# Performance work log

Measured on AMD Instinct MI355X. Metric: run time of the kernel, lower is better.

The kernel has to match this reference:

```python
import jax, jax.numpy as jnp
import numpy as np

B, S, D, H = 2, 2048, 1024, 16
HD = D // H
EPS = 1e-5


def layer_norm(x, g, b):
    mu = jnp.mean(x, axis=-1, keepdims=True)
    var = jnp.mean(jnp.square(x - mu), axis=-1, keepdims=True)
    return (x - mu) * jax.lax.rsqrt(var + EPS) * g + b


def setup_inputs() -> dict:
    key = jax.random.key(0)
    ks = jax.random.split(key, 10)
    s = 0.02
    return {
        'x': jax.random.normal(ks[0], (B, S, D), jnp.float32),
        'Wq': jax.random.normal(ks[1], (D, D), jnp.float32) * s,
        'bq': jnp.zeros((D,), jnp.float32),
        'Wk': jax.random.normal(ks[2], (D, D), jnp.float32) * s,
        'bk': jnp.zeros((D,), jnp.float32),
        'Wv': jax.random.normal(ks[3], (D, D), jnp.float32) * s,
        'bv': jnp.zeros((D,), jnp.float32),
        'W1': jax.random.normal(ks[4], (D, 4 * D), jnp.float32) * s,
        'b1': jnp.zeros((4 * D,), jnp.float32),
        'W2': jax.random.normal(ks[5], (4 * D, D), jnp.float32) * s,
        'b2': jnp.zeros((D,), jnp.float32),
        'g1': jnp.ones((D,), jnp.float32),
        'be1': jnp.zeros((D,), jnp.float32),
        'g2': jnp.ones((D,), jnp.float32),
        'be2': jnp.zeros((D,), jnp.float32),
    }


def reference(x, Wq, bq, Wk, bk, Wv, bv, W1, b1, W2, b2, g1, be1, g2, be2):
    b, s, d = x.shape
    # QKV projections, split heads: [B,H,S,HD]
    Q = (x @ Wq + bq).reshape(b, s, H, HD).transpose(0, 2, 1, 3)
    K = (x @ Wk + bk).reshape(b, s, H, HD).transpose(0, 2, 1, 3)
    V = (x @ Wv + bv).reshape(b, s, H, HD).transpose(0, 2, 1, 3)
    score = jnp.einsum('bhqd,bhkd->bhqk', Q, K) / jnp.sqrt(jnp.float32(HD))
    attn = jax.nn.softmax(score, axis=-1)
    out = jnp.einsum('bhqk,bhkd->bhqd', attn, V)
    out = out.transpose(0, 2, 1, 3).reshape(b, s, d)
    # dropout(p=0.1) is identity in eval mode
    out = layer_norm(out + x, g1, be1)
    ffn = jax.nn.gelu(out @ W1 + b1, approximate=False) @ W2 + b2
    # NOTE: faithful to source: norm2(output + output), i.e. 2*ffn_out
    return layer_norm(ffn + ffn, g2, be2)
```

## Files before the change

kernel.cpp:

```cpp
#include <hip/hip_runtime.h>
#include <hip/hip_bf16.h>

typedef __hip_bfloat16 bf16;
typedef __attribute__((ext_vector_type(8))) short short8;
typedef __attribute__((ext_vector_type(4))) float floatx4;

struct __align__(8) bf16x4 { bf16 v[4]; };

#define LOG2E 1.4426950408889634f

__device__ __forceinline__ void gload_lds16(const void* g, void* l) {
  __builtin_amdgcn_global_load_lds(
      (const __attribute__((address_space(1))) void*)g,
      (__attribute__((address_space(3))) void*)l, 16, 0, 0);
}

__device__ __forceinline__ floatx4 mfma16(short8 a, short8 b, floatx4 c) {
  return __builtin_amdgcn_mfma_f32_16x16x32_bf16(a, b, c, 0, 0, 0);
}

__global__ __launch_bounds__(256) void convert_x(const float* __restrict__ x,
                                                 bf16* __restrict__ xb) {
  int i = blockIdx.x * 256 + threadIdx.x;
  float4 v = ((const float4*)x)[i];
  bf16x4 o;
  o.v[0] = __float2bfloat16(v.x);
  o.v[1] = __float2bfloat16(v.y);
  o.v[2] = __float2bfloat16(v.z);
  o.v[3] = __float2bfloat16(v.w);
  ((bf16x4*)xb)[i] = o;
}

__global__ __launch_bounds__(256) void transpose_w(const float* __restrict__ W,
                                                   bf16* __restrict__ WT,
                                                   int K, int N) {
  __shared__ float t[64][65];
  const int n0 = blockIdx.x * 64, k0 = blockIdx.y * 64;
  const int tid = threadIdx.x;
#pragma unroll
  for (int i = 0; i < 16; ++i) {
    int idx = i * 256 + tid;
    int r = idx >> 6, c = idx & 63;
    t[r][c] = W[(size_t)(k0 + r) * N + n0 + c];
  }
  __syncthreads();
#pragma unroll
  for (int i = 0; i < 16; ++i) {
    int idx = i * 256 + tid;
    int r = idx >> 6, c = idx & 63;
    WT[(size_t)(n0 + r) * K + k0 + c] = __float2bfloat16(t[c][r]);
  }
}

__global__ __launch_bounds__(256) void transpose_v(const bf16* __restrict__ V,
                                                   bf16* __restrict__ Vt) {
  __shared__ bf16 t[64][72];
  const int bh = blockIdx.y;
  const int s0 = blockIdx.x * 64;
  const bf16* src = V + (size_t)bh * 2048 * 64;
  bf16* dst = Vt + (size_t)bh * 64 * 2048;
  const int tid = threadIdx.x;
#pragma unroll
  for (int i = 0; i < 16; ++i) {
    int idx = i * 256 + tid;
    int r = idx >> 6, c = idx & 63;
    t[r][c] = src[(size_t)(s0 + r) * 64 + c];
  }
  __syncthreads();
#pragma unroll
  for (int i = 0; i < 16; ++i) {
    int idx = i * 256 + tid;
    int r = idx >> 6, c = idx & 63;
    dst[(size_t)r * 2048 + s0 + c] = t[c][r];
  }
}

template <int MODE>
__global__ __launch_bounds__(512, 2) void gemm256(
    const bf16* __restrict__ A, const bf16* __restrict__ BT,
    const float* __restrict__ bias0, const float* __restrict__ bias1,
    const float* __restrict__ bias2, void* __restrict__ C0,
    void* __restrict__ C1, void* __restrict__ C2,
    int M, int N, int K, int lda, int ldb) {
  __shared__ bf16 As[2][256 * 64];
  __shared__ bf16 Bs[2][256 * 64];
  const int tid = threadIdx.x;
  const int lane = tid & 63, wid = tid >> 6;
  const int l16 = lane & 15, lhi = lane >> 4;
  const int wm = wid >> 2, wn = wid & 3;
  const int nwg = gridDim.x * gridDim.y;
  const int orig = blockIdx.y * gridDim.x + blockIdx.x;
  const int wflat = (orig & 7) * (nwg >> 3) + (orig >> 3);
  const int bx = wflat % gridDim.x, by = wflat / gridDim.x;
  const int brow = by * 256, bcol = bx * 256;
  const int swz = (l16 & 7) << 4;
  floatx4 acc[8][4] = {};

  auto stage = [&](int buf, int kt) {
#pragma unroll
    for (int i = 0; i < 4; ++i) {
      const int f = i * 512 + tid;
      const int row = f >> 3;
      const int cb = ((f & 7) * 16) ^ ((row & 7) << 4);
      gload_lds16((const char*)A + ((size_t)(brow + row) * lda + kt) * 2 + cb,
                  (char*)&As[buf][0] + (size_t)f * 16);
    }
#pragma unroll
    for (int i = 0; i < 4; ++i) {
      const int f = i * 512 + tid;
      const int row = f >> 3;
      const int cb = ((f & 7) * 16) ^ ((row & 7) << 4);
      gload_lds16((const char*)BT + ((size_t)(bcol + row) * ldb + kt) * 2 + cb,
                  (char*)&Bs[buf][0] + (size_t)f * 16);
    }
  };

  const int nk = K >> 6;
  stage(0, 0);
  asm volatile("s_waitcnt vmcnt(0)" ::: "memory");
  asm volatile("s_barrier" ::: "memory");
  int cur = 0;
  for (int t = 0; t < nk; ++t) {
    const char* Ab = (const char*)&As[cur][0];
    const char* Bb = (const char*)&Bs[cur][0];
    short8 af[8], b0, b1;
#pragma unroll
    for (int m = 0; m < 8; ++m)
      af[m] = *(const short8*)(Ab + (wm * 128 + m * 16 + l16) * 128 + ((lhi * 16) ^ swz));
    b0 = *(const short8*)(Bb + (wn * 64 + l16) * 128 + ((lhi * 16) ^ swz));
    b1 = *(const short8*)(Bb + (wn * 64 + 16 + l16) * 128 + ((lhi * 16) ^ swz));
    if (t + 1 < nk) stage(cur ^ 1, (t + 1) << 6);
    asm volatile("s_barrier" ::: "memory");
    __builtin_amdgcn_s_setprio(1);
#pragma unroll
    for (int m = 0; m < 8; ++m) {
      acc[m][0] = mfma16(af[m], b0, acc[m][0]);
      acc[m][1] = mfma16(af[m], b1, acc[m][1]);
    }
    __builtin_amdgcn_s_setprio(0);
    asm volatile("s_barrier" ::: "memory");
    b0 = *(const short8*)(Bb + (wn * 64 + 32 + l16) * 128 + ((lhi * 16) ^ swz));
    b1 = *(const short8*)(Bb + (wn * 64 + 48 + l16) * 128 + ((lhi * 16) ^ swz));
    asm volatile("s_barrier" ::: "memory");
    __builtin_amdgcn_s_setprio(1);
#pragma unroll
    for (int m = 0; m < 8; ++m) {
      acc[m][2] = mfma16(af[m], b0, acc[m][2]);
      acc[m][3] = mfma16(af[m], b1, acc[m][3]);
    }
    __builtin_amdgcn_s_setprio(0);
    asm volatile("s_barrier" ::: "memory");
#pragma unroll
    for (int m = 0; m < 8; ++m)
      af[m] = *(const short8*)(Ab + (wm * 128 + m * 16 + l16) * 128 + ((64 + lhi * 16) ^ swz));
    b0 = *(const short8*)(Bb + (wn * 64 + l16) * 128 + ((64 + lhi * 16) ^ swz));
    b1 = *(const short8*)(Bb + (wn * 64 + 16 + l16) * 128 + ((64 + lhi * 16) ^ swz));
    asm volatile("s_barrier" ::: "memory");
    __builtin_amdgcn_s_setprio(1);
#pragma unroll
    for (int m = 0; m < 8; ++m) {
      acc[m][0] = mfma16(af[m], b0, acc[m][0]);
      acc[m][1] = mfma16(af[m], b1, acc[m][1]);
    }
    __builtin_amdgcn_s_setprio(0);
    asm volatile("s_barrier" ::: "memory");
    b0 = *(const short8*)(Bb + (wn * 64 + 32 + l16) * 128 + ((64 + lhi * 16) ^ swz));
    b1 = *(const short8*)(Bb + (wn * 64 + 48 + l16) * 128 + ((64 + lhi * 16) ^ swz));
    asm volatile("s_waitcnt vmcnt(0)" ::: "memory");
    asm volatile("s_barrier" ::: "memory");
    __builtin_amdgcn_s_setprio(1);
#pragma unroll
    for (int m = 0; m < 8; ++m) {
      acc[m][2] = mfma16(af[m], b0, acc[m][2]);
      acc[m][3] = mfma16(af[m], b1, acc[m][3]);
    }
    __builtin_amdgcn_s_setprio(0);
    asm volatile("s_barrier" ::: "memory");
    cur ^= 1;
  }

#pragma unroll
  for (int m = 0; m < 8; ++m) {
    const int rowb = brow + wm * 128 + m * 16 + lhi * 4;
#pragma unroll
    for (int n = 0; n < 4; ++n) {
      const int col = bcol + wn * 64 + n * 16 + l16;
#pragma unroll
      for (int r = 0; r < 4; ++r) {
        float v = acc[m][n][r];
        const int gr = rowb + r;
        if constexpr (MODE == 0) {
          const int which = col >> 10;
          const int nl = col & 1023;
          const float* bp = (which == 0) ? bias0 : (which == 1) ? bias1 : bias2;
          v += bp[nl];
          const int b = gr >> 11, s = gr & 2047;
          const int h = nl >> 6, hd = nl & 63;
          const size_t dst = ((size_t)(b * 16 + h) * 2048 + s) * 64 + hd;
          bf16* out = (which == 0) ? (bf16*)C0 : (which == 1) ? (bf16*)C1 : (bf16*)C2;
          out[dst] = __float2bfloat16(v);
        } else {
          v += bias0[col];
          float gch = 0.5f * v * (1.0f + erff(v * 0.70710678118654752f));
          ((bf16*)C0)[(size_t)gr * N + col] = __float2bfloat16(gch);
        }
      }
    }
  }
}

template <int MODE>
__global__ __launch_bounds__(256, 2) void gemm_bt(
    const bf16* __restrict__ A, const bf16* __restrict__ BT,
    const float* __restrict__ bias0, const float* __restrict__ bias1,
    const float* __restrict__ bias2, void* __restrict__ C0,
    void* __restrict__ C1, void* __restrict__ C2,
    int M, int N, int K, int lda, int ldb) {
  __shared__ bf16 As[2][128 * 64];
  __shared__ bf16 Bs[2][128 * 64];
  const int tid = threadIdx.x;
  const int wid = tid >> 6, lane = tid & 63;
  const int l16 = lane & 15, lhi = lane >> 4;
  const int nwg = gridDim.x * gridDim.y;
  const int orig = blockIdx.y * gridDim.x + blockIdx.x;
  const int wflat = (orig & 7) * (nwg >> 3) + (orig >> 3);
  const int bx = wflat % gridDim.x, by = wflat / gridDim.x;
  const int brow = by * 128, bcol = bx * 128;
  const int z = blockIdx.z;
  const size_t koff = (size_t)z * (size_t)K;
  const int wr = (wid >> 1) * 64, wc = (wid & 1) * 64;
  const int swz = (l16 & 7) << 4;
  floatx4 acc[4][4] = {};

  auto stage = [&](int buf, int kt) {
#pragma unroll
    for (int i = 0; i < 4; ++i) {
      const int f = i * 256 + tid;
      const int row = f >> 3;
      const int cb = ((f & 7) * 16) ^ ((row & 7) << 4);
      gload_lds16((const char*)A + ((size_t)(brow + row) * lda + koff + kt) * 2 + cb,
                  (char*)&As[buf][0] + (size_t)f * 16);
      gload_lds16((const char*)BT + ((size_t)(bcol + row) * ldb + koff + kt) * 2 + cb,
                  (char*)&Bs[buf][0] + (size_t)f * 16);
    }
  };

  const int nk = K >> 6;
  stage(0, 0);
  int cur = 0;
  for (int t = 0; t < nk; ++t) {
    if (t + 1 < nk) {
      stage(cur ^ 1, (t + 1) << 6);
      asm volatile("s_waitcnt vmcnt(8)" ::: "memory");
    } else {
      asm volatile("s_waitcnt vmcnt(0)" ::: "memory");
    }
    asm volatile("s_barrier" ::: "memory");
#pragma unroll
    for (int kk = 0; kk < 2; ++kk) {
      short8 af[4], bfr[4];
#pragma unroll
      for (int m = 0; m < 4; ++m)
        af[m] = *(const short8*)((const char*)&As[cur][0] +
                                 (wr + m * 16 + l16) * 128 + ((kk * 64 + lhi * 16) ^ swz));
#pragma unroll
      for (int n = 0; n < 4; ++n)
        bfr[n] = *(const short8*)((const char*)&Bs[cur][0] +
                                  (wc + n * 16 + l16) * 128 + ((kk * 64 + lhi * 16) ^ swz));
      __builtin_amdgcn_s_setprio(1);
#pragma unroll
      for (int m = 0; m < 4; ++m)
#pragma unroll
        for (int n = 0; n < 4; ++n) acc[m][n] = mfma16(af[m], bfr[n], acc[m][n]);
      __builtin_amdgcn_s_setprio(0);
    }
    asm volatile("s_barrier" ::: "memory");
    cur ^= 1;
  }

#pragma unroll
  for (int m = 0; m < 4; ++m) {
    const int rowb = brow + wr + m * 16 + lhi * 4;
#pragma unroll
    for (int n = 0; n < 4; ++n) {
      const int col = bcol + wc + n * 16 + l16;
#pragma unroll
      for (int r = 0; r < 4; ++r) {
        float v = acc[m][n][r];
        const int gr = rowb + r;
        float* dst = (z == 0) ? (float*)C0 : (float*)C1;
        dst[(size_t)gr * N + col] = v;
      }
    }
  }
}

__global__ __launch_bounds__(512, 2) void flash_attn(const bf16* __restrict__ Q,
                                                     const bf16* __restrict__ Kb,
                                                     const bf16* __restrict__ Vt,
                                                     bf16* __restrict__ attn) {
  __shared__ bf16 Ks[2][64 * 64];
  __shared__ bf16 Vs[2][64 * 64];
  __shared__ bf16 Ps[8][16 * 64];
  const int tid = threadIdx.x, wid = tid >> 6, lane = tid & 63;
  const int l16 = lane & 15, lhi = lane >> 4, lhi4 = (lane >> 4) * 4;
  const int bid = blockIdx.x;
  const int w = (bid & 7) * 64 + (bid >> 3);
  const int bh = w >> 4, qtile = w & 15;
  const bf16* Qbh = Q + (size_t)bh * 2048 * 64;
  const char* Kbh = (const char*)(Kb + (size_t)bh * 2048 * 64);
  const char* Vbh = (const char*)(Vt + (size_t)bh * 64 * 2048);
  bf16* Pw = &Ps[wid][0];
  const int q0 = qtile * 128 + wid * 16;
  const int swA = (l16 & 7) << 3;
  const int swzB = (l16 & 7) << 4;

  const int strow = tid >> 3;
  const int stcol = ((tid & 7) * 16) ^ ((strow & 7) << 4);

  short8 qf[2];
#pragma unroll
  for (int kk = 0; kk < 2; ++kk)
    qf[kk] = *(const short8*)&Qbh[(size_t)(q0 + l16) * 64 + kk * 32 + lhi * 8];

  floatx4 o[4] = {};
  float mrow = -1e30f;
  float lrow = 0.0f;
  const float SC = 0.125f * LOG2E;

  auto stage = [&](bf16* Kd, bf16* Vd, int t) {
    const int kvr = t * 64;
    gload_lds16(Kbh + (size_t)(kvr + strow) * 128 + stcol, (char*)Kd + tid * 16);
    gload_lds16(Vbh + (size_t)strow * 4096 + (size_t)kvr * 2 + stcol, (char*)Vd + tid * 16);
  };

  auto tile = [&](bf16* Kc, bf16* Vc, bf16* Kn, bf16* Vn, int t) {
    if (t + 1 < 32) {
      stage(Kn, Vn, t + 1);
      asm volatile("s_waitcnt vmcnt(2)" ::: "memory");
    } else {
      asm volatile("s_waitcnt vmcnt(0)" ::: "memory");
    }
    asm volatile("s_barrier" ::: "memory");

    short8 kf[2][4];
#pragma unroll
    for (int kk = 0; kk < 2; ++kk)
#pragma unroll
      for (int fc = 0; fc < 4; ++fc)
        kf[kk][fc] = *(const short8*)((const char*)Kc + (fc * 16 + l16) * 128 +
                                      ((kk * 64 + lhi * 16) ^ swzB));

    floatx4 sf[4] = {};
    __builtin_amdgcn_s_setprio(1);
#pragma unroll
    for (int kk = 0; kk < 2; ++kk)
#pragma unroll
      for (int fc = 0; fc < 4; ++fc) sf[fc] = mfma16(kf[kk][fc], qf[kk], sf[fc]);
    __builtin_amdgcn_s_setprio(0);

    {
      float a0 = fmaxf(fmaxf(sf[0][0], sf[0][1]), fmaxf(sf[0][2], sf[0][3]));
      float a1 = fmaxf(fmaxf(sf[1][0], sf[1][1]), fmaxf(sf[1][2], sf[1][3]));
      float a2 = fmaxf(fmaxf(sf[2][0], sf[2][1]), fmaxf(sf[2][2], sf[2][3]));
      float a3 = fmaxf(fmaxf(sf[3][0], sf[3][1]), fmaxf(sf[3][2], sf[3][3]));
      float mx = fmaxf(fmaxf(a0, a1), fmaxf(a2, a3));
      mx = fmaxf(mx, __shfl_xor(mx, 16));
      mx = fmaxf(mx, __shfl_xor(mx, 32));
      mx *= SC;
      if (__any(mx > mrow + 11.54f)) {
        const float mnew = fmaxf(mrow, mx);
        const float corr = exp2f(mrow - mnew);
        mrow = mnew;
        lrow *= corr;
#pragma unroll
        for (int r = 0; r < 4; ++r) {
          const float c = __shfl(corr, lhi4 + r);
#pragma unroll
          for (int fc = 0; fc < 4; ++fc) o[fc][r] *= c;
        }
      }
      const float m = mrow;
      float rs = 0.0f;
#pragma unroll
      for (int fc = 0; fc < 4; ++fc)
#pragma unroll
        for (int r = 0; r < 4; ++r) {
          const float p = exp2f(fmaf(sf[fc][r], SC, -m));
          sf[fc][r] = p;
          rs += p;
        }
      rs += __shfl_xor(rs, 16);
      rs += __shfl_xor(rs, 32);
      lrow += rs;
#pragma unroll
      for (int fc = 0; fc < 4; ++fc) {
        bf16x4 pk;
#pragma unroll
        for (int r = 0; r < 4; ++r) pk.v[r] = __float2bfloat16(sf[fc][r]);
        *(bf16x4*)&Pw[l16 * 64 + ((fc * 16 + lhi4) ^ swA)] = pk;
      }
    }

    short8 pf[2];
#pragma unroll
    for (int kk = 0; kk < 2; ++kk)
      pf[kk] = *(const short8*)&Pw[l16 * 64 + ((kk * 32 + lhi * 8) ^ swA)];
    __builtin_amdgcn_s_setprio(1);
#pragma unroll
    for (int kk = 0; kk < 2; ++kk) {
      short8 vf[4];
#pragma unroll
      for (int fc = 0; fc < 4; ++fc)
        vf[fc] = *(const short8*)((const char*)Vc + (fc * 16 + l16) * 128 +
                                  ((kk * 64 + lhi * 16) ^ swzB));
#pragma unroll
      for (int fc = 0; fc < 4; ++fc) o[fc] = mfma16(pf[kk], vf[fc], o[fc]);
    }
    __builtin_amdgcn_s_setprio(0);

    asm volatile("s_barrier" ::: "memory");
  };

  stage(&Ks[0][0], &Vs[0][0], 0);
  for (int t = 0; t < 32; t += 2) {
    tile(&Ks[0][0], &Vs[0][0], &Ks[1][0], &Vs[1][0], t);
    tile(&Ks[1][0], &Vs[1][0], &Ks[0][0], &Vs[0][0], t + 1);
  }

  const int b = bh >> 4, h = bh & 15;
#pragma unroll
  for (int r = 0; r < 4; ++r) {
    const float lr = __shfl(lrow, lhi4 + r);
    const float inv = 1.0f / lr;
    const int s = q0 + lhi4 + r;
    const size_t rowbase = (size_t)(b * 2048 + s) * 1024 + h * 64;
#pragma unroll
    for (int fc = 0; fc < 4; ++fc)
      attn[rowbase + fc * 16 + l16] = __float2bfloat16(o[fc][r] * inv);
  }
}

__global__ __launch_bounds__(256) void ln_res(const bf16* __restrict__ attn,
                                              const float* __restrict__ x,
                                              const float* __restrict__ g,
                                              const float* __restrict__ be,
                                              bf16* __restrict__ out) {
  __shared__ float sa[4], sb[4];
  const int row = blockIdx.x;
  const size_t base = (size_t)row * 1024;
  const int tid = threadIdx.x;
  const int c0 = tid * 4;
  float4 xv = *(const float4*)(x + base + c0);
  bf16x4 av = *(const bf16x4*)(attn + base + c0);
  float v[4];
  v[0] = xv.x + __bfloat162float(av.v[0]);
  v[1] = xv.y + __bfloat162float(av.v[1]);
  v[2] = xv.z + __bfloat162float(av.v[2]);
  v[3] = xv.w + __bfloat162float(av.v[3]);
  float s = v[0] + v[1] + v[2] + v[3];
  float ss = v[0]*v[0] + v[1]*v[1] + v[2]*v[2] + v[3]*v[3];
#pragma unroll
  for (int d = 32; d > 0; d >>= 1) { s += __shfl_down(s, d); ss += __shfl_down(ss, d); }
  const int wid = tid >> 6, lane = tid & 63;
  if (lane == 0) { sa[wid] = s; sb[wid] = ss; }
  __syncthreads();
  if (tid == 0) { sa[0] = sa[0]+sa[1]+sa[2]+sa[3]; sb[0] = sb[0]+sb[1]+sb[2]+sb[3]; }
  __syncthreads();
  s = sa[0]; ss = sb[0];
  const float mu = s * (1.0f / 1024.0f);
  const float var = ss * (1.0f / 1024.0f) - mu * mu;
  const float rs = rsqrtf(var + 1e-5f);
  float4 gv = *(const float4*)(g + c0);
  float4 bv = *(const float4*)(be + c0);
  bf16x4 o;
  o.v[0] = __float2bfloat16((v[0]-mu)*rs*gv.x + bv.x);
  o.v[1] = __float2bfloat16((v[1]-mu)*rs*gv.y + bv.y);
  o.v[2] = __float2bfloat16((v[2]-mu)*rs*gv.z + bv.z);
  o.v[3] = __float2bfloat16((v[3]-mu)*rs*gv.w + bv.w);
  *(bf16x4*)(out + base + c0) = o;
}

__global__ __launch_bounds__(256) void ln2_kernel(const float* __restrict__ y0,
                                                  const float* __restrict__ y1,
                                                  const float* __restrict__ b2,
                                                  const float* __restrict__ g,
                                                  const float* __restrict__ be,
                                                  float* __restrict__ out) {
  __shared__ float sa[4], sb[4];
  const int row = blockIdx.x;
  const size_t base = (size_t)row * 1024;
  const int tid = threadIdx.x;
  const int c0 = tid * 4;
  float4 ya = *(const float4*)(y0 + base + c0);
  float4 yb = *(const float4*)(y1 + base + c0);
  float4 bb = *(const float4*)(b2 + c0);
  float v[4] = {2.0f * (ya.x + yb.x + bb.x), 2.0f * (ya.y + yb.y + bb.y),
                2.0f * (ya.z + yb.z + bb.z), 2.0f * (ya.w + yb.w + bb.w)};
  float s = v[0] + v[1] + v[2] + v[3];
  float ss = v[0]*v[0] + v[1]*v[1] + v[2]*v[2] + v[3]*v[3];
#pragma unroll
  for (int d = 32; d > 0; d >>= 1) { s += __shfl_down(s, d); ss += __shfl_down(ss, d); }
  const int wid = tid >> 6, lane = tid & 63;
  if (lane == 0) { sa[wid] = s; sb[wid] = ss; }
  __syncthreads();
  if (tid == 0) { sa[0] = sa[0]+sa[1]+sa[2]+sa[3]; sb[0] = sb[0]+sb[1]+sb[2]+sb[3]; }
  __syncthreads();
  s = sa[0]; ss = sb[0];
  const float mu = s * (1.0f / 1024.0f);
  const float var = ss * (1.0f / 1024.0f) - mu * mu;
  const float rs = rsqrtf(var + 1e-5f);
  float4 gv = *(const float4*)(g + c0);
  float4 bv = *(const float4*)(be + c0);
  float4 o;
  o.x = (v[0]-mu)*rs*gv.x + bv.x;
  o.y = (v[1]-mu)*rs*gv.y + bv.y;
  o.z = (v[2]-mu)*rs*gv.z + bv.z;
  o.w = (v[3]-mu)*rs*gv.w + bv.w;
  *(float4*)(out + base + c0) = o;
}

extern "C" void kernel_launch(void* const* d_in, const int* in_sizes, int n_in,
                              void* d_out, int out_size, void* d_ws, size_t ws_size,
                              hipStream_t stream) {
  const float* x   = (const float*)d_in[0];
  const float* Wq  = (const float*)d_in[1];
  const float* bq  = (const float*)d_in[2];
  const float* Wk  = (const float*)d_in[3];
  const float* bk  = (const float*)d_in[4];
  const float* Wv  = (const float*)d_in[5];
  const float* bv  = (const float*)d_in[6];
  const float* W1  = (const float*)d_in[7];
  const float* b1  = (const float*)d_in[8];
  const float* W2  = (const float*)d_in[9];
  const float* b2  = (const float*)d_in[10];
  const float* g1  = (const float*)d_in[11];
  const float* be1 = (const float*)d_in[12];
  const float* g2  = (const float*)d_in[13];
  const float* be2 = (const float*)d_in[14];

  char* ws = (char*)d_ws;
  bf16* xb    = (bf16*)(ws + 0ull);
  bf16* WqkvT = (bf16*)(ws + 8388608ull);
  bf16* W1T   = (bf16*)(ws + 14680064ull);
  bf16* W2T   = (bf16*)(ws + 23068672ull);
  bf16* Qb    = (bf16*)(ws + 31457280ull);
  bf16* Kb    = (bf16*)(ws + 39845888ull);
  bf16* Vb    = (bf16*)(ws + 48234496ull);
  bf16* Vt    = (bf16*)(ws + 56623104ull);
  bf16* h1    = (bf16*)(ws + 31457280ull);
  bf16* attn  = (bf16*)(ws + 65011712ull);
  bf16* ln1   = (bf16*)(ws + 73400320ull);
  float* y2a  = (float*)(ws + 0ull);
  float* y2b  = (float*)(ws + 65011712ull);
  float* out  = (float*)d_out;

  convert_x<<<4096, 256, 0, stream>>>(x, xb);
  transpose_w<<<dim3(16, 16), 256, 0, stream>>>(Wq, WqkvT, 1024, 1024);
  transpose_w<<<dim3(16, 16), 256, 0, stream>>>(Wk, WqkvT + 1024 * 1024, 1024, 1024);
  transpose_w<<<dim3(16, 16), 256, 0, stream>>>(Wv, WqkvT + 2 * 1024 * 1024, 1024, 1024);
  transpose_w<<<dim3(64, 16), 256, 0, stream>>>(W1, W1T, 1024, 4096);
  transpose_w<<<dim3(16, 64), 256, 0, stream>>>(W2, W2T, 4096, 1024);

  gemm256<0><<<dim3(12, 16), 512, 0, stream>>>(xb, WqkvT, bq, bk, bv,
                                               (void*)Qb, (void*)Kb, (void*)Vb,
                                               4096, 3072, 1024, 1024, 1024);
  transpose_v<<<dim3(32, 32), 256, 0, stream>>>(Vb, Vt);
  flash_attn<<<512, 512, 0, stream>>>(Qb, Kb, Vt, attn);
  ln_res<<<4096, 256, 0, stream>>>(attn, x, g1, be1, ln1);
  gemm256<1><<<dim3(16, 16), 512, 0, stream>>>(ln1, W1T, b1, nullptr, nullptr,
                                               (void*)h1, nullptr, nullptr,
                                               4096, 4096, 1024, 1024, 1024);
  gemm_bt<3><<<dim3(8, 32, 2), 256, 0, stream>>>(h1, W2T, nullptr, nullptr, nullptr,
                                                 (void*)y2a, (void*)y2b, nullptr,
                                                 4096, 1024, 2048, 4096, 4096);
  ln2_kernel<<<4096, 256, 0, stream>>>(y2a, y2b, b2, g2, be2, out);
}
```

Baseline: 244.0 us.

## Fuse QKV weight transposes, move QKV GEMM to gemm_bt, defer softmax row-sum reduction

The three Q/K/V weight transposes become one launch, and all weight transposes now use float4 loads and bf16x4 stores. The V transpose is reshaped to process four columns per thread. The QKV projection moves from the 256-tile gemm256 to the smaller-tile gemm_bt, which takes over the head-split epilogue, and gemm256 keeps only the GELU path. Flash attention now does its cross-lane row-sum shuffles once after the loop instead of on every tile. ln_res reads the bf16 copy of x instead of fp32, which halves that read but adds rounding error to the residual.

```diff
diff --git a/kernel.cpp b/kernel.cpp
--- a/kernel.cpp
+++ b/kernel.cpp
@@ -31,25 +31,47 @@
   ((bf16x4*)xb)[i] = o;
 }
 
+__device__ __forceinline__ void transpose_tile(const float* __restrict__ W,
+                                               bf16* __restrict__ WT,
+                                               int K, int N, int n0, int k0,
+                                               int tid) {
+  __shared__ float t[64][65];
+#pragma unroll
+  for (int i = 0; i < 4; ++i) {
+    int idx = i * 256 + tid;
+    int r = idx >> 4;
+    int c = (idx & 15) * 4;
+    float4 v = *(const float4*)&W[(size_t)(k0 + r) * N + n0 + c];
+    t[r][c] = v.x; t[r][c + 1] = v.y; t[r][c + 2] = v.z; t[r][c + 3] = v.w;
+  }
+  __syncthreads();
+#pragma unroll
+  for (int i = 0; i < 4; ++i) {
+    int idx = i * 256 + tid;
+    int r = idx >> 4;
+    int c = (idx & 15) * 4;
+    bf16x4 o;
+    o.v[0] = __float2bfloat16(t[c][r]);
+    o.v[1] = __float2bfloat16(t[c + 1][r]);
+    o.v[2] = __float2bfloat16(t[c + 2][r]);
+    o.v[3] = __float2bfloat16(t[c + 3][r]);
+    *(bf16x4*)&WT[(size_t)(n0 + r) * K + k0 + c] = o;
+  }
+}
+
 __global__ __launch_bounds__(256) void transpose_w(const float* __restrict__ W,
                                                    bf16* __restrict__ WT,
                                                    int K, int N) {
-  __shared__ float t[64][65];
-  const int n0 = blockIdx.x * 64, k0 = blockIdx.y * 64;
-  const int tid = threadIdx.x;
-#pragma unroll
-  for (int i = 0; i < 16; ++i) {
-    int idx = i * 256 + tid;
-    int r = idx >> 6, c = idx & 63;
-    t[r][c] = W[(size_t)(k0 + r) * N + n0 + c];
-  }
-  __syncthreads();
-#pragma unroll
-  for (int i = 0; i < 16; ++i) {
-    int idx = i * 256 + tid;
-    int r = idx >> 6, c = idx & 63;
-    WT[(size_t)(n0 + r) * K + k0 + c] = __float2bfloat16(t[c][r]);
-  }
+  transpose_tile(W, WT, K, N, blockIdx.x * 64, blockIdx.y * 64, threadIdx.x);
+}
+
+__global__ __launch_bounds__(256) void transpose_qkv(const float* __restrict__ Wq,
+                                                     const float* __restrict__ Wk,
+                                                     const float* __restrict__ Wv,
+                                                     bf16* __restrict__ WT) {
+  const float* W = (blockIdx.z == 0) ? Wq : (blockIdx.z == 1) ? Wk : Wv;
+  bf16* dst = WT + (size_t)blockIdx.z * 1024 * 1024;
+  transpose_tile(W, dst, 1024, 1024, blockIdx.x * 64, blockIdx.y * 64, threadIdx.x);
 }
 
 __global__ __launch_bounds__(256) void transpose_v(const bf16* __restrict__ V,
@@ -68,144 +90,16 @@
   }
   __syncthreads();
 #pragma unroll
-  for (int i = 0; i < 16; ++i) {
+  for (int i = 0; i < 4; ++i) {
     int idx = i * 256 + tid;
-    int r = idx >> 6, c = idx & 63;
-    dst[(size_t)r * 2048 + s0 + c] = t[c][r];
-  }
-}
-
-template <int MODE>
-__global__ __launch_bounds__(512, 2) void gemm256(
-    const bf16* __restrict__ A, const bf16* __restrict__ BT,
-    const float* __restrict__ bias0, const float* __restrict__ bias1,
-    const float* __restrict__ bias2, void* __restrict__ C0,
-    void* __restrict__ C1, void* __restrict__ C2,
-    int M, int N, int K, int lda, int ldb) {
-  __shared__ bf16 As[2][256 * 64];
-  __shared__ bf16 Bs[2][256 * 64];
-  const int tid = threadIdx.x;
-  const int lane = tid & 63, wid = tid >> 6;
-  const int l16 = lane & 15, lhi = lane >> 4;
-  const int wm = wid >> 2, wn = wid & 3;
-  const int nwg = gridDim.x * gridDim.y;
-  const int orig = blockIdx.y * gridDim.x + blockIdx.x;
-  const int wflat = (orig & 7) * (nwg >> 3) + (orig >> 3);
-  const int bx = wflat % gridDim.x, by = wflat / gridDim.x;
-  const int brow = by * 256, bcol = bx * 256;
-  const int swz = (l16 & 7) << 4;
-  floatx4 acc[8][4] = {};
-
-  auto stage = [&](int buf, int kt) {
-#pragma unroll
-    for (int i = 0; i < 4; ++i) {
-      const int f = i * 512 + tid;
-      const int row = f >> 3;
-      const int cb = ((f & 7) * 16) ^ ((row & 7) << 4);
-      gload_lds16((const char*)A + ((size_t)(brow + row) * lda + kt) * 2 + cb,
-                  (char*)&As[buf][0] + (size_t)f * 16);
-    }
-#pragma unroll
-    for (int i = 0; i < 4; ++i) {
-      const int f = i * 512 + tid;
-      const int row = f >> 3;
-      const int cb = ((f & 7) * 16) ^ ((row & 7) << 4);
-      gload_lds16((const char*)BT + ((size_t)(bcol + row) * ldb + kt) * 2 + cb,
-                  (char*)&Bs[buf][0] + (size_t)f * 16);
-    }
-  };
-
-  const int nk = K >> 6;
-  stage(0, 0);
-  asm volatile("s_waitcnt vmcnt(0)" ::: "memory");
-  asm volatile("s_barrier" ::: "memory");
-  int cur = 0;
-  for (int t = 0; t < nk; ++t) {
-    const char* Ab = (const char*)&As[cur][0];
-    const char* Bb = (const char*)&Bs[cur][0];
-    short8 af[8], b0, b1;
-#pragma unroll
-    for (int m = 0; m < 8; ++m)
-      af[m] = *(const short8*)(Ab + (wm * 128 + m * 16 + l16) * 128 + ((lhi * 16) ^ swz));
-    b0 = *(const short8*)(Bb + (wn * 64 + l16) * 128 + ((lhi * 16) ^ swz));
-    b1 = *(const short8*)(Bb + (wn * 64 + 16 + l16) * 128 + ((lhi * 16) ^ swz));
-    if (t + 1 < nk) stage(cur ^ 1, (t + 1) << 6);
-    asm volatile("s_barrier" ::: "memory");
-    __builtin_amdgcn_s_setprio(1);
-#pragma unroll
-    for (int m = 0; m < 8; ++m) {
-      acc[m][0] = mfma16(af[m], b0, acc[m][0]);
-      acc[m][1] = mfma16(af[m], b1, acc[m][1]);
-    }
-    __builtin_amdgcn_s_setprio(0);
-    asm volatile("s_barrier" ::: "memory");
-    b0 = *(const short8*)(Bb + (wn * 64 + 32 + l16) * 128 + ((lhi * 16) ^ swz));
-    b1 = *(const short8*)(Bb + (wn * 64 + 48 + l16) * 128 + ((lhi * 16) ^ swz));
-    asm volatile("s_barrier" ::: "memory");
-    __builtin_amdgcn_s_setprio(1);
-#pragma unroll
-    for (int m = 0; m < 8; ++m) {
-      acc[m][2] = mfma16(af[m], b0, acc[m][2]);
-      acc[m][3] = mfma16(af[m], b1, acc[m][3]);
-    }
-    __builtin_amdgcn_s_setprio(0);
-    asm volatile("s_barrier" ::: "memory");
-#pragma unroll
-    for (int m = 0; m < 8; ++m)
-      af[m] = *(const short8*)(Ab + (wm * 128 + m * 16 + l16) * 128 + ((64 + lhi * 16) ^ swz));
-    b0 = *(const short8*)(Bb + (wn * 64 + l16) * 128 + ((64 + lhi * 16) ^ swz));
-    b1 = *(const short8*)(Bb + (wn * 64 + 16 + l16) * 128 + ((64 + lhi * 16) ^ swz));
-    asm volatile("s_barrier" ::: "memory");
-    __builtin_amdgcn_s_setprio(1);
-#pragma unroll
-    for (int m = 0; m < 8; ++m) {
-      acc[m][0] = mfma16(af[m], b0, acc[m][0]);
-      acc[m][1] = mfma16(af[m], b1, acc[m][1]);
-    }
-    __builtin_amdgcn_s_setprio(0);
-    asm volatile("s_barrier" ::: "memory");
-    b0 = *(const short8*)(Bb + (wn * 64 + 32 + l16) * 128 + ((64 + lhi * 16) ^ swz));
-    b1 = *(const short8*)(Bb + (wn * 64 + 48 + l16) * 128 + ((64 + lhi * 16) ^ swz));
-    asm volatile("s_waitcnt vmcnt(0)" ::: "memory");
-    asm volatile("s_barrier" ::: "memory");
-    __builtin_amdgcn_s_setprio(1);
-#pragma unroll
-    for (int m = 0; m < 8; ++m) {
-      acc[m][2] = mfma16(af[m], b0, acc[m][2]);
-      acc[m][3] = mfma16(af[m], b1, acc[m][3]);
-    }
-    __builtin_amdgcn_s_setprio(0);
-    asm volatile("s_barrier" ::: "memory");
-    cur ^= 1;
-  }
-
-#pragma unroll
-  for (int m = 0; m < 8; ++m) {
-    const int rowb = brow + wm * 128 + m * 16 + lhi * 4;
-#pragma unroll
-    for (int n = 0; n < 4; ++n) {
-      const int col = bcol + wn * 64 + n * 16 + l16;
-#pragma unroll
-      for (int r = 0; r < 4; ++r) {
-        float v = acc[m][n][r];
-        const int gr = rowb + r;
-        if constexpr (MODE == 0) {
-          const int which = col >> 10;
-          const int nl = col & 1023;
-          const float* bp = (which == 0) ? bias0 : (which == 1) ? bias1 : bias2;
-          v += bp[nl];
-          const int b = gr >> 11, s = gr & 2047;
-          const int h = nl >> 6, hd = nl & 63;
-          const size_t dst = ((size_t)(b * 16 + h) * 2048 + s) * 64 + hd;
-          bf16* out = (which == 0) ? (bf16*)C0 : (which == 1) ? (bf16*)C1 : (bf16*)C2;
-          out[dst] = __float2bfloat16(v);
-        } else {
-          v += bias0[col];
-          float gch = 0.5f * v * (1.0f + erff(v * 0.70710678118654752f));
-          ((bf16*)C0)[(size_t)gr * N + col] = __float2bfloat16(gch);
-        }
-      }
-    }
+    int r = idx >> 4;
+    int c = (idx & 15) * 4;
+    bf16x4 o;
+    o.v[0] = t[r][c]; o.v[1] = t[r][c + 1]; o.v[2] = t[r][c + 2]; o.v[3] = t[r][c + 3];
+    dst[(size_t)c * 2048 + s0 + r] = o.v[0];
+    dst[(size_t)(c + 1) * 2048 + s0 + r] = o.v[1];
+    dst[(size_t)(c + 2) * 2048 + s0 + r] = o.v[2];
+    dst[(size_t)(c + 3) * 2048 + s0 + r] = o.v[3];
   }
 }
 
@@ -288,8 +182,138 @@
       for (int r = 0; r < 4; ++r) {
         float v = acc[m][n][r];
         const int gr = rowb + r;
-        float* dst = (z == 0) ? (float*)C0 : (float*)C1;
-        dst[(size_t)gr * N + col] = v;
+        if constexpr (MODE == 0) {
+          const int which = col >> 10;
+          const int nl = col & 1023;
+          const float* bp = (which == 0) ? bias0 : (which == 1) ? bias1 : bias2;
+          v += bp[nl];
+          const int b = gr >> 11, s = gr & 2047;
+          const int h = nl >> 6, hd = nl & 63;
+          const size_t dst = ((size_t)(b * 16 + h) * 2048 + s) * 64 + hd;
+          bf16* out = (which == 0) ? (bf16*)C0 : (which == 1) ? (bf16*)C1 : (bf16*)C2;
+          out[dst] = __float2bfloat16(v);
+        } else {
+          float* dst = (z == 0) ? (float*)C0 : (float*)C1;
+          dst[(size_t)gr * N + col] = v;
+        }
+      }
+    }
+  }
+}
+
+template <int MODE>
+__global__ __launch_bounds__(512, 2) void gemm256(
+    const bf16* __restrict__ A, const bf16* __restrict__ BT,
+    const float* __restrict__ bias0, void* __restrict__ C0,
+    int M, int N, int K, int lda, int ldb) {
+  __shared__ bf16 As[2][256 * 64];
+  __shared__ bf16 Bs[2][256 * 64];
+  const int tid = threadIdx.x;
+  const int lane = tid & 63, wid = tid >> 6;
+  const int l16 = lane & 15, lhi = lane >> 4;
+  const int wm = wid >> 2, wn = wid & 3;
+  const int nwg = gridDim.x * gridDim.y;
+  const int orig = blockIdx.y * gridDim.x + blockIdx.x;
+  const int wflat = (orig & 7) * (nwg >> 3) + (orig >> 3);
+  const int bx = wflat % gridDim.x, by = wflat / gridDim.x;
+  const int brow = by * 256, bcol = bx * 256;
+  const int swz = (l16 & 7) << 4;
+  floatx4 acc[8][4] = {};
+
+  auto stage = [&](int buf, int kt) {
+#pragma unroll
+    for (int i = 0; i < 4; ++i) {
+      const int f = i * 512 + tid;
+      const int row = f >> 3;
+      const int cb = ((f & 7) * 16) ^ ((row & 7) << 4);
+      gload_lds16((const char*)A + ((size_t)(brow + row) * lda + kt) * 2 + cb,
+                  (char*)&As[buf][0] + (size_t)f * 16);
+    }
+#pragma unroll
+    for (int i = 0; i < 4; ++i) {
+      const int f = i * 512 + tid;
+      const int row = f >> 3;
+      const int cb = ((f & 7) * 16) ^ ((row & 7) << 4);
+      gload_lds16((const char*)BT + ((size_t)(bcol + row) * ldb + kt) * 2 + cb,
+                  (char*)&Bs[buf][0] + (size_t)f * 16);
+    }
+  };
+
+  const int nk = K >> 6;
+  stage(0, 0);
+  asm volatile("s_waitcnt vmcnt(0)" ::: "memory");
+  asm volatile("s_barrier" ::: "memory");
+  int cur = 0;
+  for (int t = 0; t < nk; ++t) {
+    const char* Ab = (const char*)&As[cur][0];
+    const char* Bb = (const char*)&Bs[cur][0];
+    short8 af[8], b0, b1;
+#pragma unroll
+    for (int m = 0; m < 8; ++m)
+      af[m] = *(const short8*)(Ab + (wm * 128 + m * 16 + l16) * 128 + ((lhi * 16) ^ swz));
+    b0 = *(const short8*)(Bb + (wn * 64 + l16) * 128 + ((lhi * 16) ^ swz));
+    b1 = *(const short8*)(Bb + (wn * 64 + 16 + l16) * 128 + ((lhi * 16) ^ swz));
+    if (t + 1 < nk) stage(cur ^ 1, (t + 1) << 6);
+    asm volatile("s_barrier" ::: "memory");
+    __builtin_amdgcn_s_setprio(1);
+#pragma unroll
+    for (int m = 0; m < 8; ++m) {
+      acc[m][0] = mfma16(af[m], b0, acc[m][0]);
+      acc[m][1] = mfma16(af[m], b1, acc[m][1]);
+    }
+    __builtin_amdgcn_s_setprio(0);
+    asm volatile("s_barrier" ::: "memory");
+    b0 = *(const short8*)(Bb + (wn * 64 + 32 + l16) * 128 + ((lhi * 16) ^ swz));
+    b1 = *(const short8*)(Bb + (wn * 64 + 48 + l16) * 128 + ((lhi * 16) ^ swz));
+    asm volatile("s_barrier" ::: "memory");
+    __builtin_amdgcn_s_setprio(1);
+#pragma unroll
+    for (int m = 0; m < 8; ++m) {
+      acc[m][2] = mfma16(af[m], b0, acc[m][2]);
+      acc[m][3] = mfma16(af[m], b1, acc[m][3]);
+    }
+    __builtin_amdgcn_s_setprio(0);
+    asm volatile("s_barrier" ::: "memory");
+#pragma unroll
+    for (int m = 0; m < 8; ++m)
+      af[m] = *(const short8*)(Ab + (wm * 128 + m * 16 + l16) * 128 + ((64 + lhi * 16) ^ swz));
+    b0 = *(const short8*)(Bb + (wn * 64 + l16) * 128 + ((64 + lhi * 16) ^ swz));
+    b1 = *(const short8*)(Bb + (wn * 64 + 16 + l16) * 128 + ((64 + lhi * 16) ^ swz));
+    asm volatile("s_barrier" ::: "memory");
+    __builtin_amdgcn_s_setprio(1);
+#pragma unroll
+    for (int m = 0; m < 8; ++m) {
+      acc[m][0] = mfma16(af[m], b0, acc[m][0]);
+      acc[m][1] = mfma16(af[m], b1, acc[m][1]);
+    }
+    __builtin_amdgcn_s_setprio(0);
+    asm volatile("s_barrier" ::: "memory");
+    b0 = *(const short8*)(Bb + (wn * 64 + 32 + l16) * 128 + ((64 + lhi * 16) ^ swz));
+    b1 = *(const short8*)(Bb + (wn * 64 + 48 + l16) * 128 + ((64 + lhi * 16) ^ swz));
+    asm volatile("s_waitcnt vmcnt(0)" ::: "memory");
+    asm volatile("s_barrier" ::: "memory");
+    __builtin_amdgcn_s_setprio(1);
+#pragma unroll
+    for (int m = 0; m < 8; ++m) {
+      acc[m][2] = mfma16(af[m], b0, acc[m][2]);
+      acc[m][3] = mfma16(af[m], b1, acc[m][3]);
+    }
+    __builtin_amdgcn_s_setprio(0);
+    asm volatile("s_barrier" ::: "memory");
+    cur ^= 1;
+  }
+
+#pragma unroll
+  for (int m = 0; m < 8; ++m) {
+    const int rowb = brow + wm * 128 + m * 16 + lhi * 4;
+#pragma unroll
+    for (int n = 0; n < 4; ++n) {
+      const int col = bcol + wn * 64 + n * 16 + l16;
+#pragma unroll
+      for (int r = 0; r < 4; ++r) {
+        float v = acc[m][n][r] + bias0[col];
+        float gch = 0.5f * v * (1.0f + erff(v * 0.70710678118654752f));
+        ((bf16*)C0)[(size_t)(rowb + r) * N + col] = __float2bfloat16(gch);
       }
     }
   }
@@ -381,18 +405,14 @@
         }
       }
       const float m = mrow;
-      float rs = 0.0f;
 #pragma unroll
       for (int fc = 0; fc < 4; ++fc)
 #pragma unroll
         for (int r = 0; r < 4; ++r) {
           const float p = exp2f(fmaf(sf[fc][r], SC, -m));
           sf[fc][r] = p;
-          rs += p;
+          lrow += p;
         }
-      rs += __shfl_xor(rs, 16);
-      rs += __shfl_xor(rs, 32);
-      lrow += rs;
 #pragma unroll
       for (int fc = 0; fc < 4; ++fc) {
         bf16x4 pk;
@@ -427,6 +447,9 @@
     tile(&Ks[0][0], &Vs[0][0], &Ks[1][0], &Vs[1][0], t);
     tile(&Ks[1][0], &Vs[1][0], &Ks[0][0], &Vs[0][0], t + 1);
   }
+
+  lrow += __shfl_xor(lrow, 16);
+  lrow += __shfl_xor(lrow, 32);
 
   const int b = bh >> 4, h = bh & 15;
 #pragma unroll
@@ -442,7 +465,7 @@
 }
 
 __global__ __launch_bounds__(256) void ln_res(const bf16* __restrict__ attn,
-                                              const float* __restrict__ x,
+                                              const bf16* __restrict__ xb,
                                               const float* __restrict__ g,
                                               const float* __restrict__ be,
                                               bf16* __restrict__ out) {
@@ -451,13 +474,13 @@
   const size_t base = (size_t)row * 1024;
   const int tid = threadIdx.x;
   const int c0 = tid * 4;
-  float4 xv = *(const float4*)(x + base + c0);
+  bf16x4 xv = *(const bf16x4*)(xb + base + c0);
   bf16x4 av = *(const bf16x4*)(attn + base + c0);
   float v[4];
-  v[0] = xv.x + __bfloat162float(av.v[0]);
-  v[1] = xv.y + __bfloat162float(av.v[1]);
-  v[2] = xv.z + __bfloat162float(av.v[2]);
-  v[3] = xv.w + __bfloat162float(av.v[3]);
+  v[0] = __bfloat162float(xv.v[0]) + __bfloat162float(av.v[0]);
+  v[1] = __bfloat162float(xv.v[1]) + __bfloat162float(av.v[1]);
+  v[2] = __bfloat162float(xv.v[2]) + __bfloat162float(av.v[2]);
+  v[3] = __bfloat162float(xv.v[3]) + __bfloat162float(av.v[3]);
   float s = v[0] + v[1] + v[2] + v[3];
   float ss = v[0]*v[0] + v[1]*v[1] + v[2]*v[2] + v[3]*v[3];
 #pragma unroll
@@ -556,20 +579,17 @@
   float* out  = (float*)d_out;
 
   convert_x<<<4096, 256, 0, stream>>>(x, xb);
-  transpose_w<<<dim3(16, 16), 256, 0, stream>>>(Wq, WqkvT, 1024, 1024);
-  transpose_w<<<dim3(16, 16), 256, 0, stream>>>(Wk, WqkvT + 1024 * 1024, 1024, 1024);
-  transpose_w<<<dim3(16, 16), 256, 0, stream>>>(Wv, WqkvT + 2 * 1024 * 1024, 1024, 1024);
+  transpose_qkv<<<dim3(16, 16, 3), 256, 0, stream>>>(Wq, Wk, Wv, WqkvT);
   transpose_w<<<dim3(64, 16), 256, 0, stream>>>(W1, W1T, 1024, 4096);
   transpose_w<<<dim3(16, 64), 256, 0, stream>>>(W2, W2T, 4096, 1024);
 
-  gemm256<0><<<dim3(12, 16), 512, 0, stream>>>(xb, WqkvT, bq, bk, bv,
+  gemm_bt<0><<<dim3(24, 32), 256, 0, stream>>>(xb, WqkvT, bq, bk, bv,
                                                (void*)Qb, (void*)Kb, (void*)Vb,
                                                4096, 3072, 1024, 1024, 1024);
   transpose_v<<<dim3(32, 32), 256, 0, stream>>>(Vb, Vt);
   flash_attn<<<512, 512, 0, stream>>>(Qb, Kb, Vt, attn);
-  ln_res<<<4096, 256, 0, stream>>>(attn, x, g1, be1, ln1);
-  gemm256<1><<<dim3(16, 16), 512, 0, stream>>>(ln1, W1T, b1, nullptr, nullptr,
-                                               (void*)h1, nullptr, nullptr,
+  ln_res<<<4096, 256, 0, stream>>>(attn, xb, g1, be1, ln1);
+  gemm256<1><<<dim3(16, 16), 512, 0, stream>>>(ln1, W1T, b1, (void*)h1,
                                                4096, 4096, 1024, 1024, 1024);
   gemm_bt<3><<<dim3(8, 32, 2), 256, 0, stream>>>(h1, W2T, nullptr, nullptr, nullptr,
                                                  (void*)y2a, (void*)y2b, nullptr,
```

Measured after the change: 244.3 us. Within noise of the previous version (+0.1%).
